# Performance work log

Hardware: AMD Instinct MI355X
Metric: run time of the kernel (lower is better)

## Reference

```python
import math
import jax, jax.numpy as jnp
import numpy as np
from jax import lax

B, C, O, K, WDIM, H, W = 8, 512, 512, 3, 512, 64, 64
CONV_SCALE = 1.0 / math.sqrt(C * K * K)
MOD_SCALE = 1.0 / math.sqrt(WDIM)


def setup_inputs() -> dict:
    key = jax.random.key(0)
    k1, k2, k3, k4 = jax.random.split(key, 4)
    return {
        "x": jax.random.normal(k1, (B, C, H, W), dtype=jnp.float32),
        "w": jax.random.normal(k2, (B, WDIM), dtype=jnp.float32),
        "base_weight": jax.random.normal(k3, (1, O, C, K, K), dtype=jnp.float32),
        "mod_weight": jax.random.normal(k4, (C, WDIM), dtype=jnp.float32),
        "mod_bias": jnp.zeros((C,), dtype=jnp.float32),
    }


def reference(x, w, base_weight, mod_weight, mod_bias):
    # EqualLinear modulation: s in (B, C), then +1
    s = w @ (mod_weight * MOD_SCALE).T + mod_bias + 1.0  # (B, C)
    # Per-sample modulated weights: (B, O, C, K, K)
    weight = CONV_SCALE * base_weight * s[:, None, :, None, None]
    # Demodulation
    d = lax.rsqrt(jnp.sum(weight * weight, axis=(2, 3, 4), keepdims=True))
    weight = weight * d
    pad = K // 2

    def conv_one(xi, wi):
        # xi: (C, H, W), wi: (O, C, K, K)
        return lax.conv_general_dilated(
            xi[None], wi, window_strides=(1, 1),
            padding=[(pad, pad), (pad, pad)],
            dimension_numbers=("NCHW", "OIHW", "NCHW"),
        )[0]

    return jax.vmap(conv_one)(x, weight)  # (B, O, H, W)
```

## Files before the change

kernel.cpp:

```cpp
#include <hip/hip_runtime.h>
#include <stdint.h>


#define MOD_SCALE  0.044194173824159216f
#define CONV_SCALE 0.014731391274719739f

typedef __attribute__((ext_vector_type(4))) float f32x4;
typedef __attribute__((ext_vector_type(8))) short bf16x8;

__device__ inline unsigned short f2bf(float f) {
  uint32_t u = __float_as_uint(f);
  uint32_t r = (u + 0x7fffu + ((u >> 16) & 1u)) >> 16;
  return (unsigned short)r;
}

__device__ inline void gload_lds16(const void* g, void* l) {
  __builtin_amdgcn_global_load_lds(
      (const __attribute__((address_space(1))) void*)g,
      (__attribute__((address_space(3))) void*)l, 16, 0, 0);
}

__global__ __launch_bounds__(256) void k_style(const float* __restrict__ w,
                                               const float* __restrict__ modw,
                                               const float* __restrict__ modb,
                                               float* __restrict__ s_out) {
  __shared__ float red[256];
  const int tid = threadIdx.x;
  const int sb = blockIdx.x;
  const int cb = sb & 7, b = sb >> 3;
  const int cl = tid >> 2, qq = tid & 3;
  const int c = (cb << 6) + cl;
  const float4* wd = (const float4*)(w + (b << 9) + (qq << 7));
  const float4* md = (const float4*)(modw + ((size_t)c << 9) + (qq << 7));
  float acc = 0.f;
#pragma unroll
  for (int i = 0; i < 32; ++i) {
    float4 a = wd[i], m = md[i];
    acc += a.x * m.x + a.y * m.y + a.z * m.z + a.w * m.w;
  }
  red[tid] = acc;
  __syncthreads();
  if (tid < 64) {
    float v = red[tid * 4] + red[tid * 4 + 1] + red[tid * 4 + 2] + red[tid * 4 + 3];
    int cc = (cb << 6) + tid;
    s_out[(b << 9) + cc] = v * MOD_SCALE + modb[cc] + 1.0f;
  }
}

__global__ __launch_bounds__(256) void k_prep(const float* __restrict__ x,
                                              const float* __restrict__ s,
                                              unsigned short* __restrict__ xp) {
  __shared__ uint32_t tb[64 * 260];
  const int blk = blockIdx.x;
  const int tid = threadIdx.x;
  if (blk < 512) {
    const int b = blk >> 6, y = blk & 63;
    const int px4 = tid & 15;
    const int cp  = tid >> 4;
    const float* xb = x + (size_t)(b << 9) * 4096 + (y << 6) + (px4 << 2);
    const float* sb = s + (b << 9);
#pragma unroll
    for (int it = 0; it < 16; ++it) {
      const int cpair = cp + (it << 4);
      const int c0 = cpair << 1;
      const float4 a0 = *(const float4*)(xb + (size_t)c0 * 4096);
      const float4 a1 = *(const float4*)(xb + (size_t)(c0 + 1) * 4096);
      const float s0 = sb[c0], s1 = sb[c0 + 1];
      const int pxb = px4 << 2;
      tb[(pxb + 0) * 260 + cpair] = (uint32_t)f2bf(a0.x * s0) | ((uint32_t)f2bf(a1.x * s1) << 16);
      tb[(pxb + 1) * 260 + cpair] = (uint32_t)f2bf(a0.y * s0) | ((uint32_t)f2bf(a1.y * s1) << 16);
      tb[(pxb + 2) * 260 + cpair] = (uint32_t)f2bf(a0.z * s0) | ((uint32_t)f2bf(a1.z * s1) << 16);
      tb[(pxb + 3) * 260 + cpair] = (uint32_t)f2bf(a0.w * s0) | ((uint32_t)f2bf(a1.w * s1) << 16);
    }
    __syncthreads();
    const int wv = tid >> 6, l = tid & 63;
    uint32_t* xpw = (uint32_t*)xp;
#pragma unroll
    for (int it = 0; it < 16; ++it) {
      const int px = (wv << 4) + it;
      const uint4 v = *(const uint4*)(tb + px * 260 + (l << 2));
      const size_t base = ((size_t)b * 4356 + (size_t)(y + 1) * 66 + (px + 1)) << 8;
      ((uint4*)(xpw + base))[l] = v;
    }
  } else {
    const int q = blk - 512;
    const int b = q / 260, p = q - b * 260;
    int py, px;
    if (p < 66)       { py = 0;       px = p; }
    else if (p < 132) { py = 65;      px = p - 66; }
    else if (p < 196) { py = p - 131; px = 0; }
    else              { py = p - 195; px = 65; }
    uint32_t* dst = (uint32_t*)(xp + ((size_t)b * 4356 + py * 66 + px) * 512);
    dst[tid] = 0u;
  }
}

__global__ __launch_bounds__(256) void k_fwd(const float* __restrict__ bw,
                                             const float* __restrict__ s,
                                             unsigned short* __restrict__ awT,
                                             float* __restrict__ d_out) {
  __shared__ float lw[4608];
  __shared__ float ls[4096];
  __shared__ float red[32];
  const int tid = threadIdx.x;
  const int o = blockIdx.x;
  {
    const float4* src = (const float4*)(bw + (size_t)o * 4608);
    float4* dst = (float4*)lw;
#pragma unroll
    for (int i = 0; i < 4; ++i) dst[tid + (i << 8)] = src[tid + (i << 8)];
    if (tid < 128) dst[tid + 1024] = src[tid + 1024];
  }
  {
    const float4* src = (const float4*)s;
    float4* dst = (float4*)ls;
#pragma unroll
    for (int i = 0; i < 4; ++i) dst[tid + (i << 8)] = src[tid + (i << 8)];
  }
  __syncthreads();
  const int c0 = tid << 1;
  const int base = c0 * 9;
  float wq0 = 0.f, wq1 = 0.f;
#pragma unroll
  for (int j = 0; j < 9; ++j) {
    float a = lw[base + j];      wq0 += a * a;
    float b2 = lw[base + 9 + j]; wq1 += b2 * b2;
  }
  const int lane = tid & 63, wv = tid >> 6;
#pragma unroll
  for (int b = 0; b < 8; ++b) {
    float s0 = ls[(b << 9) + c0], s1 = ls[(b << 9) + c0 + 1];
    float v = wq0 * s0 * s0 + wq1 * s1 * s1;
#pragma unroll
    for (int off = 32; off > 0; off >>= 1) v += __shfl_down(v, off, 64);
    if (lane == 0) red[(b << 2) + wv] = v;
  }
  __syncthreads();
  if (tid < 8) {
    float a = red[tid << 2] + red[(tid << 2) + 1] + red[(tid << 2) + 2] + red[(tid << 2) + 3];
    d_out[(tid << 9) + o] = rsqrtf(a * (1.0f / 4608.0f)) * CONV_SCALE;
  }
  uint32_t* dst = (uint32_t*)(awT + (size_t)o * 4608);
#pragma unroll
  for (int j = 0; j < 9; ++j)
    dst[(j << 8) + tid] = (uint32_t)f2bf(lw[base + j]) |
                          ((uint32_t)f2bf(lw[base + 9 + j]) << 16);
}

__global__ __launch_bounds__(256, 2) void k_conv(const unsigned short* __restrict__ awT,
                                                 const unsigned short* __restrict__ xpad,
                                                 const float* __restrict__ dmod,
                                                 float* __restrict__ out) {
  __shared__ alignas(16) unsigned short As[3 * 8192];
  __shared__ alignas(16) unsigned short Bs[8448];
  const int tid = threadIdx.x;
  const int b  = blockIdx.z;
  const int m0 = blockIdx.y << 7;
  const int n0 = blockIdx.x << 7;
  const int y0 = n0 >> 6;

  const int srow = tid >> 3;
  const int schk = ((tid & 7) - (srow & 7)) & 7;
  const int scol = schk << 3;

  const unsigned short* A0 = awT + (size_t)(m0 + srow) * 4608 + scol;
  const size_t bx = (size_t)b * (66 * 66 * 512);

  const int lane = tid & 63;
  const int wv   = tid >> 6;
  const int moff = (wv >> 1) << 6;
  const int noff = (wv & 1) << 6;
  const int noffp = noff ? 66 : 0;
  const int lm   = lane & 15;
  const int g4   = lane >> 4;

  const unsigned short* ardA[2];
#pragma unroll
  for (int h = 0; h < 2; ++h)
    ardA[h] = As + (moff + lm) * 64 + ((((h << 2) + g4) + moff + lm) & 7) * 8;
  const unsigned short* ardB[3][2];
#pragma unroll
  for (int kx = 0; kx < 3; ++kx) {
    const int rb = noffp + lm + kx;
#pragma unroll
    for (int h = 0; h < 2; ++h)
      ardB[kx][h] = Bs + rb * 64 + ((((h << 2) + g4) + rb) & 7) * 8;
  }

  f32x4 acc[4][4];
#pragma unroll
  for (int i = 0; i < 4; ++i)
#pragma unroll
    for (int j = 0; j < 4; ++j) acc[i][j] = (f32x4){0.f, 0.f, 0.f, 0.f};

#pragma unroll 1
  for (int ky = 0; ky < 3; ++ky) {
    const unsigned short* Bp0 = xpad + bx + (size_t)((y0 + ky) * 66 + srow) * 512 + scol;
#pragma unroll 1
    for (int kb = 0; kb < 8; ++kb) {
      const int kcol = kb << 6;
#pragma unroll
      for (int kx = 0; kx < 3; ++kx) {
        const unsigned short* Ap = A0 + ((ky * 3 + kx) << 9) + kcol;
#pragma unroll
        for (int g = 0; g < 4; ++g)
          gload_lds16(Ap + g * (32 * 4608), As + ((kx << 13) + (((g << 8) + tid) << 3)));
      }
      const unsigned short* Bp = Bp0 + kcol;
#pragma unroll
      for (int g = 0; g < 4; ++g)
        gload_lds16(Bp + g * (32 * 512), Bs + (((g << 8) + tid) << 3));
      if (tid < 32) gload_lds16(Bp + 128 * 512, Bs + 8192 + tid * 8);
      __syncthreads();
#pragma unroll
      for (int kx = 0; kx < 3; ++kx) {
#pragma unroll
        for (int h = 0; h < 2; ++h) {
          bf16x8 af[4], bf[4];
          const unsigned short* pa = ardA[h] + (kx << 13);
          const unsigned short* pb = ardB[kx][h];
#pragma unroll
          for (int i = 0; i < 4; ++i) af[i] = *(const bf16x8*)(pa + (i << 10));
#pragma unroll
          for (int j = 0; j < 4; ++j) bf[j] = *(const bf16x8*)(pb + (j << 10));
#pragma unroll
          for (int i = 0; i < 4; ++i)
#pragma unroll
            for (int j = 0; j < 4; ++j)
              acc[i][j] = __builtin_amdgcn_mfma_f32_16x16x32_bf16(af[i], bf[j], acc[i][j], 0, 0, 0);
        }
      }
      __syncthreads();
    }
  }

  const float* dB = dmod + (b << 9) + m0 + moff;
  float* op = out + (size_t)((b << 9) + m0 + moff) * 4096 + n0 + noff;
#pragma unroll
  for (int i = 0; i < 4; ++i) {
#pragma unroll
    for (int r = 0; r < 4; ++r) {
      const int m = i * 16 + (g4 << 2) + r;
      const float dm = dB[m];
#pragma unroll
      for (int j = 0; j < 4; ++j)
        op[(size_t)m * 4096 + (j << 4) + lm] = acc[i][j][r] * dm;
    }
  }
}

extern "C" void kernel_launch(void* const* d_in, const int* in_sizes, int n_in,
                              void* d_out, int out_size, void* d_ws, size_t ws_size,
                              hipStream_t stream) {
  const float* x    = (const float*)d_in[0];
  const float* w    = (const float*)d_in[1];
  const float* bw   = (const float*)d_in[2];
  const float* modw = (const float*)d_in[3];
  const float* modb = (const float*)d_in[4];
  float* out = (float*)d_out;
  char* ws = (char*)d_ws;

  float* s_buf = (float*)(ws);
  float* d_buf = (float*)(ws + 16384);
  unsigned short* awT  = (unsigned short*)(ws + 32768);
  unsigned short* xpad = (unsigned short*)(ws + 4751360);

  (void)in_sizes; (void)n_in; (void)out_size; (void)ws_size;

  k_style<<<64,   256, 0, stream>>>(w, modw, modb, s_buf);
  k_fwd  <<<512,  256, 0, stream>>>(bw, s_buf, awT, d_buf);
  k_prep <<<2592, 256, 0, stream>>>(x, s_buf, xpad);
  k_conv <<<dim3(32, 4, 8), 256, 0, stream>>>(awT, xpad, d_buf, out);
}
```

Before: 258.7 us.

## Halve conv K-tile to 32 channels to fit four blocks per CU

```diff
diff --git a/kernel.cpp b/kernel.cpp
--- a/kernel.cpp
+++ b/kernel.cpp
@@ -147,24 +147,25 @@
                           ((uint32_t)f2bf(lw[base + 9 + j]) << 16);
 }
 
-__global__ __launch_bounds__(256, 2) void k_conv(const unsigned short* __restrict__ awT,
+__global__ __launch_bounds__(256, 4) void k_conv(const unsigned short* __restrict__ awT,
                                                  const unsigned short* __restrict__ xpad,
                                                  const float* __restrict__ dmod,
                                                  float* __restrict__ out) {
-  __shared__ alignas(16) unsigned short As[3 * 8192];
-  __shared__ alignas(16) unsigned short Bs[8448];
+  __shared__ alignas(16) unsigned short As[3 * 4096];
+  __shared__ alignas(16) unsigned short Bs[4224];
   const int tid = threadIdx.x;
   const int b  = blockIdx.z;
   const int m0 = blockIdx.y << 7;
   const int n0 = blockIdx.x << 7;
   const int y0 = n0 >> 6;
 
-  const int srow = tid >> 3;
-  const int schk = ((tid & 7) - (srow & 7)) & 7;
-  const int scol = schk << 3;
-
-  const unsigned short* A0 = awT + (size_t)(m0 + srow) * 4608 + scol;
-  const size_t bx = (size_t)b * (66 * 66 * 512);
+  const int srow4 = tid >> 2;
+  const int sl    = ((tid & 3) - (tid >> 3)) & 3;
+  const int scol  = sl << 3;
+
+  const unsigned short* A0 = awT + (size_t)(m0 + srow4) * 4608 + scol;
+  const unsigned short* B0 = xpad + (size_t)b * (66 * 66 * 512)
+                                  + (size_t)(y0 * 66 + srow4) * 512 + scol;
 
   const int lane = tid & 63;
   const int wv   = tid >> 6;
@@ -174,17 +175,13 @@
   const int lm   = lane & 15;
   const int g4   = lane >> 4;
 
-  const unsigned short* ardA[2];
-#pragma unroll
-  for (int h = 0; h < 2; ++h)
-    ardA[h] = As + (moff + lm) * 64 + ((((h << 2) + g4) + moff + lm) & 7) * 8;
-  const unsigned short* ardB[3][2];
+  const int arow = moff + lm;
+  const int aoff = arow * 32 + (((g4 + (arow >> 1)) & 3) << 3);
+  int boff[3];
 #pragma unroll
   for (int kx = 0; kx < 3; ++kx) {
     const int rb = noffp + lm + kx;
-#pragma unroll
-    for (int h = 0; h < 2; ++h)
-      ardB[kx][h] = Bs + rb * 64 + ((((h << 2) + g4) + rb) & 7) * 8;
+    boff[kx] = rb * 32 + (((g4 + (rb >> 1)) & 3) << 3);
   }
 
   f32x4 acc[4][4];
@@ -195,41 +192,40 @@
 
 #pragma unroll 1
   for (int ky = 0; ky < 3; ++ky) {
-    const unsigned short* Bp0 = xpad + bx + (size_t)((y0 + ky) * 66 + srow) * 512 + scol;
 #pragma unroll 1
-    for (int kb = 0; kb < 8; ++kb) {
-      const int kcol = kb << 6;
+    for (int kb = 0; kb < 16; ++kb) {
+      const int kcol = kb << 5;
 #pragma unroll
       for (int kx = 0; kx < 3; ++kx) {
         const unsigned short* Ap = A0 + ((ky * 3 + kx) << 9) + kcol;
 #pragma unroll
-        for (int g = 0; g < 4; ++g)
-          gload_lds16(Ap + g * (32 * 4608), As + ((kx << 13) + (((g << 8) + tid) << 3)));
+        for (int g = 0; g < 2; ++g)
+          gload_lds16(Ap + (size_t)(g << 6) * 4608,
+                      As + (kx << 12) + (((g << 8) + tid) << 3));
       }
-      const unsigned short* Bp = Bp0 + kcol;
-#pragma unroll
-      for (int g = 0; g < 4; ++g)
-        gload_lds16(Bp + g * (32 * 512), Bs + (((g << 8) + tid) << 3));
-      if (tid < 32) gload_lds16(Bp + 128 * 512, Bs + 8192 + tid * 8);
+      const unsigned short* Bp = B0 + (size_t)(ky * 66) * 512 + kcol;
+#pragma unroll
+      for (int g = 0; g < 2; ++g)
+        gload_lds16(Bp + (size_t)(g << 6) * 512, Bs + (((g << 8) + tid) << 3));
+      if (tid < 16) gload_lds16(Bp + (size_t)128 * 512, Bs + ((512 + tid) << 3));
       __syncthreads();
+      __builtin_amdgcn_s_setprio(1);
 #pragma unroll
       for (int kx = 0; kx < 3; ++kx) {
-#pragma unroll
-        for (int h = 0; h < 2; ++h) {
-          bf16x8 af[4], bf[4];
-          const unsigned short* pa = ardA[h] + (kx << 13);
-          const unsigned short* pb = ardB[kx][h];
-#pragma unroll
-          for (int i = 0; i < 4; ++i) af[i] = *(const bf16x8*)(pa + (i << 10));
-#pragma unroll
-          for (int j = 0; j < 4; ++j) bf[j] = *(const bf16x8*)(pb + (j << 10));
-#pragma unroll
-          for (int i = 0; i < 4; ++i)
-#pragma unroll
-            for (int j = 0; j < 4; ++j)
-              acc[i][j] = __builtin_amdgcn_mfma_f32_16x16x32_bf16(af[i], bf[j], acc[i][j], 0, 0, 0);
-        }
+        bf16x8 af[4], bf[4];
+        const unsigned short* pa = As + (kx << 12) + aoff;
+        const unsigned short* pb = Bs + boff[kx];
+#pragma unroll
+        for (int i = 0; i < 4; ++i) af[i] = *(const bf16x8*)(pa + (i << 9));
+#pragma unroll
+        for (int j = 0; j < 4; ++j) bf[j] = *(const bf16x8*)(pb + (j << 9));
+#pragma unroll
+        for (int i = 0; i < 4; ++i)
+#pragma unroll
+          for (int j = 0; j < 4; ++j)
+            acc[i][j] = __builtin_amdgcn_mfma_f32_16x16x32_bf16(af[i], bf[j], acc[i][j], 0, 0, 0);
       }
+      __builtin_amdgcn_s_setprio(0);
       __syncthreads();
     }
   }
```

After: 280.5 us. +8.5%, slower.

## Stream conv weights directly to registers and double-buffer input tiles in LDS

Applied to the files above, without the earlier changes.

```diff
diff --git a/kernel.cpp b/kernel.cpp
--- a/kernel.cpp
+++ b/kernel.cpp
@@ -151,19 +151,22 @@
                                                  const unsigned short* __restrict__ xpad,
                                                  const float* __restrict__ dmod,
                                                  float* __restrict__ out) {
-  __shared__ alignas(16) unsigned short As[3 * 8192];
-  __shared__ alignas(16) unsigned short Bs[8448];
-  const int tid = threadIdx.x;
-  const int b  = blockIdx.z;
-  const int m0 = blockIdx.y << 7;
-  const int n0 = blockIdx.x << 7;
-  const int y0 = n0 >> 6;
+  __shared__ alignas(16) unsigned short Bs[2][8448];
+  const int tid = threadIdx.x;
+
+  const int bid = blockIdx.x;
+  const int g   = bid & 7;
+  const int k   = bid >> 3;
+  const int nI  = k & 31;
+  const int zq  = k >> 5;
+  const int b   = (zq << 1) | (g >> 2);
+  const int m0  = (g & 3) << 7;
+  const int n0  = nI << 7;
+  const int y0  = n0 >> 6;
 
   const int srow = tid >> 3;
   const int schk = ((tid & 7) - (srow & 7)) & 7;
   const int scol = schk << 3;
-
-  const unsigned short* A0 = awT + (size_t)(m0 + srow) * 4608 + scol;
   const size_t bx = (size_t)b * (66 * 66 * 512);
 
   const int lane = tid & 63;
@@ -174,18 +177,16 @@
   const int lm   = lane & 15;
   const int g4   = lane >> 4;
 
-  const unsigned short* ardA[2];
-#pragma unroll
-  for (int h = 0; h < 2; ++h)
-    ardA[h] = As + (moff + lm) * 64 + ((((h << 2) + g4) + moff + lm) & 7) * 8;
-  const unsigned short* ardB[3][2];
+  int boff[3][2];
 #pragma unroll
   for (int kx = 0; kx < 3; ++kx) {
     const int rb = noffp + lm + kx;
 #pragma unroll
     for (int h = 0; h < 2; ++h)
-      ardB[kx][h] = Bs + rb * 64 + ((((h << 2) + g4) + rb) & 7) * 8;
-  }
+      boff[kx][h] = rb * 64 + ((((h << 2) + g4) + rb) & 7) * 8;
+  }
+
+  const unsigned short* aBase = awT + (size_t)(m0 + moff + lm) * 4608 + (g4 << 3);
 
   f32x4 acc[4][4];
 #pragma unroll
@@ -193,46 +194,66 @@
 #pragma unroll
     for (int j = 0; j < 4; ++j) acc[i][j] = (f32x4){0.f, 0.f, 0.f, 0.f};
 
+  bf16x8 a0[2][4], a1[2][4], a2[2][4];
+
+  auto stageB = [&](int buf, int it) {
+    const int ky = it >> 3, kcol = (it & 7) << 6;
+    const unsigned short* Bp = xpad + bx + (size_t)((y0 + ky) * 66 + srow) * 512 + scol + kcol;
+#pragma unroll
+    for (int gg = 0; gg < 4; ++gg)
+      gload_lds16(Bp + gg * (32 * 512), &Bs[buf][((gg << 8) + tid) << 3]);
+    if (tid < 32) gload_lds16(Bp + 128 * 512, &Bs[buf][8192 + tid * 8]);
+  };
+
+  auto loadA = [&](bf16x8 (&dst)[2][4], int it, int kx) {
+    const int ky = it >> 3, kcol = (it & 7) << 6;
+    const unsigned short* ap = aBase + ((ky * 3 + kx) << 9) + kcol;
+#pragma unroll
+    for (int h = 0; h < 2; ++h)
+#pragma unroll
+      for (int i = 0; i < 4; ++i)
+        dst[h][i] = *(const bf16x8*)(ap + (h << 5) + (size_t)i * 73728);
+  };
+
+  auto mfmaKX = [&](const bf16x8 (&af)[2][4], const unsigned short* Bb, const int (&bo)[2]) {
+    __builtin_amdgcn_s_setprio(1);
+#pragma unroll
+    for (int h = 0; h < 2; ++h) {
+      bf16x8 bfr[4];
+      const unsigned short* pb = Bb + bo[h];
+#pragma unroll
+      for (int j = 0; j < 4; ++j) bfr[j] = *(const bf16x8*)(pb + (j << 10));
+#pragma unroll
+      for (int i = 0; i < 4; ++i)
+#pragma unroll
+        for (int j = 0; j < 4; ++j)
+          acc[i][j] = __builtin_amdgcn_mfma_f32_16x16x32_bf16(af[h][i], bfr[j], acc[i][j], 0, 0, 0);
+    }
+    __builtin_amdgcn_s_setprio(0);
+  };
+
+  stageB(0, 0);
+  loadA(a0, 0, 0);
+  __syncthreads();
+
+  int cur = 0;
 #pragma unroll 1
-  for (int ky = 0; ky < 3; ++ky) {
-    const unsigned short* Bp0 = xpad + bx + (size_t)((y0 + ky) * 66 + srow) * 512 + scol;
-#pragma unroll 1
-    for (int kb = 0; kb < 8; ++kb) {
-      const int kcol = kb << 6;
-#pragma unroll
-      for (int kx = 0; kx < 3; ++kx) {
-        const unsigned short* Ap = A0 + ((ky * 3 + kx) << 9) + kcol;
-#pragma unroll
-        for (int g = 0; g < 4; ++g)
-          gload_lds16(Ap + g * (32 * 4608), As + ((kx << 13) + (((g << 8) + tid) << 3)));
-      }
-      const unsigned short* Bp = Bp0 + kcol;
-#pragma unroll
-      for (int g = 0; g < 4; ++g)
-        gload_lds16(Bp + g * (32 * 512), Bs + (((g << 8) + tid) << 3));
-      if (tid < 32) gload_lds16(Bp + 128 * 512, Bs + 8192 + tid * 8);
-      __syncthreads();
-#pragma unroll
-      for (int kx = 0; kx < 3; ++kx) {
-#pragma unroll
-        for (int h = 0; h < 2; ++h) {
-          bf16x8 af[4], bf[4];
-          const unsigned short* pa = ardA[h] + (kx << 13);
-          const unsigned short* pb = ardB[kx][h];
-#pragma unroll
-          for (int i = 0; i < 4; ++i) af[i] = *(const bf16x8*)(pa + (i << 10));
-#pragma unroll
-          for (int j = 0; j < 4; ++j) bf[j] = *(const bf16x8*)(pb + (j << 10));
-#pragma unroll
-          for (int i = 0; i < 4; ++i)
-#pragma unroll
-            for (int j = 0; j < 4; ++j)
-              acc[i][j] = __builtin_amdgcn_mfma_f32_16x16x32_bf16(af[i], bf[j], acc[i][j], 0, 0, 0);
-        }
-      }
-      __syncthreads();
-    }
-  }
+  for (int it = 0; it < 23; ++it) {
+    loadA(a1, it, 1);
+    stageB(cur ^ 1, it + 1);
+    mfmaKX(a0, Bs[cur], boff[0]);
+    loadA(a2, it, 2);
+    mfmaKX(a1, Bs[cur], boff[1]);
+    loadA(a0, it + 1, 0);
+    mfmaKX(a2, Bs[cur], boff[2]);
+    __syncthreads();
+    cur ^= 1;
+  }
+  loadA(a1, 23, 1);
+  mfmaKX(a0, Bs[cur], boff[0]);
+  loadA(a2, 23, 2);
+  mfmaKX(a1, Bs[cur], boff[1]);
+  mfmaKX(a2, Bs[cur], boff[2]);
 
   const float* dB = dmod + (b << 9) + m0 + moff;
   float* op = out + (size_t)((b << 9) + m0 + moff) * 4096 + n0 + noff;
@@ -270,5 +291,5 @@
   k_style<<<64,   256, 0, stream>>>(w, modw, modb, s_buf);
   k_fwd  <<<512,  256, 0, stream>>>(bw, s_buf, awT, d_buf);
   k_prep <<<2592, 256, 0, stream>>>(x, s_buf, xpad);
-  k_conv <<<dim3(32, 4, 8), 256, 0, stream>>>(awT, xpad, d_buf, out);
-}
+  k_conv <<<1024, 256, 0, stream>>>(awT, xpad, d_buf, out);
+}
```

Result: slower. 416.1 us (+60.9%).

## Enlarge conv GEMM tile to 256x256 with 512-thread blocks and MFMA priority

Applied to the files above, without the earlier changes.

```diff
diff --git a/kernel.cpp b/kernel.cpp
--- a/kernel.cpp
+++ b/kernel.cpp
@@ -147,17 +147,21 @@
                           ((uint32_t)f2bf(lw[base + 9 + j]) << 16);
 }
 
-__global__ __launch_bounds__(256, 2) void k_conv(const unsigned short* __restrict__ awT,
+__global__ __launch_bounds__(512, 2) void k_conv(const unsigned short* __restrict__ awT,
                                                  const unsigned short* __restrict__ xpad,
                                                  const float* __restrict__ dmod,
                                                  float* __restrict__ out) {
-  __shared__ alignas(16) unsigned short As[3 * 8192];
-  __shared__ alignas(16) unsigned short Bs[8448];
-  const int tid = threadIdx.x;
-  const int b  = blockIdx.z;
-  const int m0 = blockIdx.y << 7;
-  const int n0 = blockIdx.x << 7;
-  const int y0 = n0 >> 6;
+  __shared__ alignas(16) unsigned short As[3 * 16384];
+  __shared__ alignas(16) unsigned short Bs[16896];
+  const int tid = threadIdx.x;
+
+  const int bid = blockIdx.x;
+  const int bm  = bid & 15;
+  const int nI  = bid >> 4;
+  const int b   = bm >> 1;
+  const int m0  = (bm & 1) << 8;
+  const int n0  = nI << 8;
+  const int y0  = n0 >> 6;
 
   const int srow = tid >> 3;
   const int schk = ((tid & 7) - (srow & 7)) & 7;
@@ -165,37 +169,39 @@
 
   const unsigned short* A0 = awT + (size_t)(m0 + srow) * 4608 + scol;
   const size_t bx = (size_t)b * (66 * 66 * 512);
+  const unsigned short* B0 = xpad + bx + (size_t)(y0 * 66 + srow) * 512 + scol;
 
   const int lane = tid & 63;
   const int wv   = tid >> 6;
   const int moff = (wv >> 1) << 6;
-  const int noff = (wv & 1) << 6;
-  const int noffp = noff ? 66 : 0;
+  const int noff = (wv & 1) << 7;
   const int lm   = lane & 15;
   const int g4   = lane >> 4;
 
-  const unsigned short* ardA[2];
+  const int arow = moff + lm;
+  int aoff[2];
 #pragma unroll
   for (int h = 0; h < 2; ++h)
-    ardA[h] = As + (moff + lm) * 64 + ((((h << 2) + g4) + moff + lm) & 7) * 8;
-  const unsigned short* ardB[3][2];
-#pragma unroll
-  for (int kx = 0; kx < 3; ++kx) {
-    const int rb = noffp + lm + kx;
-#pragma unroll
-    for (int h = 0; h < 2; ++h)
-      ardB[kx][h] = Bs + rb * 64 + ((((h << 2) + g4) + rb) & 7) * 8;
-  }
-
-  f32x4 acc[4][4];
+    aoff[h] = arow * 64 + ((((h << 2) + g4) + arow) & 7) * 8;
+  int boff[3][2][2];
+#pragma unroll
+  for (int kx = 0; kx < 3; ++kx)
+#pragma unroll
+    for (int jr = 0; jr < 2; ++jr) {
+      const int rb = (wv & 1) * 132 + jr * 66 + lm + kx;
+#pragma unroll
+      for (int h = 0; h < 2; ++h)
+        boff[kx][jr][h] = rb * 64 + ((((h << 2) + g4) + rb) & 7) * 8;
+    }
+
+  f32x4 acc[4][8];
 #pragma unroll
   for (int i = 0; i < 4; ++i)
 #pragma unroll
-    for (int j = 0; j < 4; ++j) acc[i][j] = (f32x4){0.f, 0.f, 0.f, 0.f};
+    for (int j = 0; j < 8; ++j) acc[i][j] = (f32x4){0.f, 0.f, 0.f, 0.f};
 
 #pragma unroll 1
   for (int ky = 0; ky < 3; ++ky) {
-    const unsigned short* Bp0 = xpad + bx + (size_t)((y0 + ky) * 66 + srow) * 512 + scol;
 #pragma unroll 1
     for (int kb = 0; kb < 8; ++kb) {
       const int kcol = kb << 6;
@@ -204,32 +210,35 @@
         const unsigned short* Ap = A0 + ((ky * 3 + kx) << 9) + kcol;
 #pragma unroll
         for (int g = 0; g < 4; ++g)
-          gload_lds16(Ap + g * (32 * 4608), As + ((kx << 13) + (((g << 8) + tid) << 3)));
+          gload_lds16(Ap + (size_t)(g << 6) * 4608,
+                      As + (kx << 14) + (g << 12) + (tid << 3));
       }
-      const unsigned short* Bp = Bp0 + kcol;
+      const unsigned short* Bp = B0 + (size_t)(ky * 66) * 512 + kcol;
 #pragma unroll
       for (int g = 0; g < 4; ++g)
-        gload_lds16(Bp + g * (32 * 512), Bs + (((g << 8) + tid) << 3));
-      if (tid < 32) gload_lds16(Bp + 128 * 512, Bs + 8192 + tid * 8);
+        gload_lds16(Bp + (size_t)(g << 6) * 512, Bs + (g << 12) + (tid << 3));
+      if (tid < 64) gload_lds16(Bp + (size_t)256 * 512, Bs + 16384 + (tid << 3));
       __syncthreads();
+      __builtin_amdgcn_s_setprio(1);
 #pragma unroll
       for (int kx = 0; kx < 3; ++kx) {
 #pragma unroll
         for (int h = 0; h < 2; ++h) {
-          bf16x8 af[4], bf[4];
-          const unsigned short* pa = ardA[h] + (kx << 13);
-          const unsigned short* pb = ardB[kx][h];
+          bf16x8 af[4], bfr[8];
+          const unsigned short* pa = As + (kx << 14) + aoff[h];
 #pragma unroll
           for (int i = 0; i < 4; ++i) af[i] = *(const bf16x8*)(pa + (i << 10));
 #pragma unroll
-          for (int j = 0; j < 4; ++j) bf[j] = *(const bf16x8*)(pb + (j << 10));
+          for (int j = 0; j < 8; ++j)
+            bfr[j] = *(const bf16x8*)(Bs + boff[kx][j >> 2][h] + ((j & 3) << 10));
 #pragma unroll
           for (int i = 0; i < 4; ++i)
 #pragma unroll
-            for (int j = 0; j < 4; ++j)
-              acc[i][j] = __builtin_amdgcn_mfma_f32_16x16x32_bf16(af[i], bf[j], acc[i][j], 0, 0, 0);
+            for (int j = 0; j < 8; ++j)
+              acc[i][j] = __builtin_amdgcn_mfma_f32_16x16x32_bf16(af[i], bfr[j], acc[i][j], 0, 0, 0);
         }
       }
+      __builtin_amdgcn_s_setprio(0);
       __syncthreads();
     }
   }
@@ -243,7 +252,7 @@
       const int m = i * 16 + (g4 << 2) + r;
       const float dm = dB[m];
 #pragma unroll
-      for (int j = 0; j < 4; ++j)
+      for (int j = 0; j < 8; ++j)
         op[(size_t)m * 4096 + (j << 4) + lm] = acc[i][j][r] * dm;
     }
   }
@@ -270,5 +279,5 @@
   k_style<<<64,   256, 0, stream>>>(w, modw, modb, s_buf);
   k_fwd  <<<512,  256, 0, stream>>>(bw, s_buf, awT, d_buf);
   k_prep <<<2592, 256, 0, stream>>>(x, s_buf, xpad);
-  k_conv <<<dim3(32, 4, 8), 256, 0, stream>>>(awT, xpad, d_buf, out);
-}
+  k_conv <<<256,  512, 0, stream>>>(awT, xpad, d_buf, out);
+}
```

Result: slower. 279.4 us (+8.0%).
